# Kernel tuning notes

Measured on AMD Instinct MI355X. Metric: run time of the kernel, lower is better.

Reference implementation:

```python
import jax, jax.numpy as jnp
import numpy as np

N = 250_000    # total nodes across the batch of graphs
E = 2_000_000  # directed edges (no self loops)
F_IN = 3       # PROTEINS node feature dim
H = 32         # hid_channel
B = 128        # number of graphs in the batch


def _connected_components(u, v, n):
    """Weakly-connected components over selected edges via min-label propagation
    with pointer jumping. Final label = min node id in the component."""
    lab0 = jnp.arange(n, dtype=u.dtype)
    def body(state):
        lab, _ = state
        m = jnp.minimum(lab[u], lab[v])
        new = lab.at[u].min(m).at[v].min(m)
        new = jnp.minimum(new, new[new])  # pointer jumping
        return new, jnp.any(new != lab)
    lab, _ = jax.lax.while_loop(lambda s: s[1], body, (lab0, jnp.bool_(True)))
    return lab


def _gcn(h, src, dst, w, self_w, n):
    """GCN propagation D^-1/2 (A + I) D^-1/2 h with per-edge weights w and
    per-node self-loop weights self_w (gcn_norm with add_remaining_self_loops)."""
    deg = jax.ops.segment_sum(w, dst, num_segments=n) + self_w
    dis = jnp.where(deg > 0, jax.lax.rsqrt(jnp.maximum(deg, 1e-12)), 0.0)
    msg = jax.ops.segment_sum(h[src] * (dis[src] * dis[dst] * w)[:, None], dst, num_segments=n)
    return msg + h * (dis * dis * self_w)[:, None]


def _forward(x, W1, b1, w_pool, b_pool, W3, b3, Wf, bf, src, dst, batch):
    n = x.shape[0]
    ew = jnp.ones_like(src, dtype=x.dtype)
    sw = jnp.ones((n,), x.dtype)
    # conv1 + ReLU (dropout = identity in eval mode)
    x1 = jax.nn.relu(_gcn(x @ W1, src, dst, ew, sw, n) + b1)
    # ClusterPooling edge scores: sigmoid(Linear([x_i ; x_j]))
    h = x1.shape[1]
    score = jax.nn.sigmoid(x1[src] @ w_pool[:h] + x1[dst] @ w_pool[h:] + b_pool)
    sel = score > 0.5
    # contract selected edges -> clusters (unselected edges mapped to harmless (0,0))
    u = jax.lax.stop_gradient(jnp.where(sel, src, 0))
    v = jax.lax.stop_gradient(jnp.where(sel, dst, 0))
    lab = _connected_components(u, v, n)            # cluster id = representative (min) node id
    rep = lab == jnp.arange(n, dtype=lab.dtype)     # valid (non-empty) cluster slots
    repf = rep.astype(x.dtype)
    # cluster score = mean score of contracted edges; 1.0 for singleton clusters
    grp = lab[src]
    cnt = jax.ops.segment_sum(sel.astype(x.dtype), grp, num_segments=n)
    ssum = jax.ops.segment_sum(jnp.where(sel, score, jnp.zeros_like(score)), grp, num_segments=n)
    cscore = jnp.where(cnt > 0, ssum / jnp.maximum(cnt, 1.0), 1.0)
    # new cluster features = (sum of member features) * cluster score
    new_x = jax.ops.segment_sum(x1, lab, num_segments=n) * cscore[:, None]
    # relabel edges to cluster ids, coalesce (dedup) and drop self loops
    ru, rv = lab[src], lab[dst]
    order = jnp.lexsort((rv, ru))
    rus, rvs = ru[order], rv[order]
    first = jnp.concatenate([jnp.ones((1,), bool), (rus[1:] != rus[:-1]) | (rvs[1:] != rvs[:-1])])
    w = (first & (rus != rvs)).astype(x.dtype)
    # conv3 + ReLU on pooled graph (self loops only on valid cluster slots)
    x3 = jax.nn.relu(_gcn(new_x @ W3, rus, rvs, w, repf, n) + b3)
    # global mean pool over the clusters of each graph (invalid slots -> dummy seg B)
    seg = jnp.where(rep, batch, B)
    gs = jax.ops.segment_sum(x3 * repf[:, None], seg, num_segments=B + 1)[:B]
    gc = jax.ops.segment_sum(repf, seg, num_segments=B + 1)[:B]
    pooled = gs / jnp.maximum(gc, 1.0)[:, None]
    return jax.nn.sigmoid(pooled @ Wf + bf).reshape(-1)  # [B], binary task -> sigmoid + flatten


def setup_inputs() -> dict:
    key = jax.random.key(0)
    ks = jax.random.split(key, 10)
    x = jax.random.normal(ks[0], (N, F_IN), dtype=jnp.float32)
    src = jax.random.randint(ks[1], (E,), 0, N, dtype=jnp.int32)
    off = jax.random.randint(ks[2], (E,), 1, N, dtype=jnp.int32)
    dst = ((src + off) % N).astype(jnp.int32)  # no self loops
    edge_list = jnp.stack([src, dst], axis=1)  # [E, 2], forward transposes
    batch = jnp.sort(jax.random.randint(ks[3], (N,), 0, B, dtype=jnp.int32))
    W1 = jax.random.normal(ks[4], (F_IN, H), jnp.float32) * 0.5
    b1 = jnp.zeros((H,), jnp.float32)
    w_pool = jax.random.normal(ks[5], (2 * H,), jnp.float32) * 0.5
    b_pool = jnp.float32(-1.0)
    W3 = jax.random.normal(ks[6], (H, H), jnp.float32) * 0.3
    b3 = jnp.zeros((H,), jnp.float32)
    Wf = jax.random.normal(ks[7], (H, 1), jnp.float32) * 0.3
    bf = jnp.zeros((1,), jnp.float32)
    return dict(x=x, edge_list=edge_list, batch=batch, W1=W1, b1=b1,
                w_pool=w_pool, b_pool=b_pool, W3=W3, b3=b3, Wf=Wf, bf=bf)


def reference(x, edge_list, batch, W1, b1, w_pool, b_pool, W3, b3, Wf, bf):
    src, dst = edge_list[:, 0], edge_list[:, 1]
    return _forward(x, W1, b1, w_pool, b_pool, W3, b3, Wf, bf, src, dst, batch)
```

## Files before the change

### kernel.cpp

```cpp
#include <hip/hip_runtime.h>

typedef unsigned long long u64;
typedef unsigned int u32;

#define HF 32
#define TBL_BITS 22
#define TBL_SIZE (1u << TBL_BITS)
#define LP_ITERS 12
#define EMPTY_KEY 0xFFFFFFFFFFFFFFFFull
#define HSLOTS 256


__global__ void k_count(const int2* __restrict__ edges, int* __restrict__ cnt, int E) {
    int e = blockIdx.x * blockDim.x + threadIdx.x;
    if (e >= E) return;
    atomicAdd(&cnt[edges[e].y], 1);
}

__global__ void k_scan1(const int* __restrict__ cnt, int* __restrict__ row,
                        int* __restrict__ bsums, int N) {
    __shared__ int s[256];
    int tid = threadIdx.x;
    int i = blockIdx.x * 256 + tid;
    int v = (i < N) ? cnt[i] : 0;
    s[tid] = v;
    __syncthreads();
    for (int o = 1; o < 256; o <<= 1) {
        int t = (tid >= o) ? s[tid - o] : 0;
        __syncthreads();
        s[tid] += t;
        __syncthreads();
    }
    if (i < N) row[i] = s[tid] - v;
    if (tid == 255) bsums[blockIdx.x] = s[255];
}

__global__ void k_scan2(int* __restrict__ bsums, int nb) {
    __shared__ int s[1024];
    int tid = threadIdx.x;
    int v = (tid < nb) ? bsums[tid] : 0;
    s[tid] = v;
    __syncthreads();
    for (int o = 1; o < 1024; o <<= 1) {
        int t = (tid >= o) ? s[tid - o] : 0;
        __syncthreads();
        s[tid] += t;
        __syncthreads();
    }
    if (tid < nb) bsums[tid] = s[tid] - v;
}

__global__ void k_scan3(int* __restrict__ row, int* __restrict__ cursor,
                        const int* __restrict__ bsums, int N, int E) {
    int i = blockIdx.x * 256 + threadIdx.x;
    if (i < N) {
        int v = row[i] + bsums[blockIdx.x];
        row[i] = v;
        cursor[i] = v;
    }
    if (i == 0) row[N] = E;
}

__global__ void k_fill(const int2* __restrict__ edges, int* __restrict__ cursor,
                       int* __restrict__ csr_src, int E) {
    int e = blockIdx.x * blockDim.x + threadIdx.x;
    if (e >= E) return;
    int2 ed = edges[e];
    int pos = atomicAdd(&cursor[ed.y], 1);
    csr_src[pos] = ed.x;
}


__global__ void k_gather_x1(const int* __restrict__ row, const int* __restrict__ csr_src,
                            const float* __restrict__ x, const float* __restrict__ W1,
                            const float* __restrict__ b1, const float* __restrict__ wp,
                            float* __restrict__ x1, float* __restrict__ a_src,
                            float* __restrict__ a_dst, int* __restrict__ lab, int N) {
    __shared__ float w[96];
    __shared__ float wpl[64];
    __shared__ float b1l[32];
    int tid = threadIdx.x;
    if (tid < 96) w[tid] = W1[tid];
    if (tid < 64) wpl[tid] = wp[tid];
    if (tid < 32) b1l[tid] = b1[tid];
    __syncthreads();
    int t = blockIdx.x * blockDim.x + tid;
    int i = t >> 3, fg = t & 7;
    if (i >= N) return;
    int f = fg * 4;
    float wa0 = w[f + 0], wa1 = w[f + 1], wa2 = w[f + 2], wa3 = w[f + 3];
    float wb0 = w[32 + f + 0], wb1 = w[32 + f + 1], wb2 = w[32 + f + 2], wb3 = w[32 + f + 3];
    float wc0 = w[64 + f + 0], wc1 = w[64 + f + 1], wc2 = w[64 + f + 2], wc3 = w[64 + f + 3];
    int r0 = row[i], r1 = row[i + 1];
    float disI = rsqrtf((float)(r1 - r0) + 1.0f);
    float xi0 = x[3 * i + 0], xi1 = x[3 * i + 1], xi2 = x[3 * i + 2];
    float4 acc;
    acc.x = (xi0 * wa0 + xi1 * wb0 + xi2 * wc0) * disI;
    acc.y = (xi0 * wa1 + xi1 * wb1 + xi2 * wc1) * disI;
    acc.z = (xi0 * wa2 + xi1 * wb2 + xi2 * wc2) * disI;
    acc.w = (xi0 * wa3 + xi1 * wb3 + xi2 * wc3) * disI;
    for (int j = r0; j < r1; j++) {
        int s = csr_src[j];
        float s0 = x[3 * s + 0], s1 = x[3 * s + 1], s2 = x[3 * s + 2];
        int sr0 = row[s], sr1 = row[s + 1];
        float disS = rsqrtf((float)(sr1 - sr0) + 1.0f);
        acc.x += (s0 * wa0 + s1 * wb0 + s2 * wc0) * disS;
        acc.y += (s0 * wa1 + s1 * wb1 + s2 * wc1) * disS;
        acc.z += (s0 * wa2 + s1 * wb2 + s2 * wc2) * disS;
        acc.w += (s0 * wa3 + s1 * wb3 + s2 * wc3) * disS;
    }
    float4 r;
    r.x = fmaxf(disI * acc.x + b1l[f + 0], 0.0f);
    r.y = fmaxf(disI * acc.y + b1l[f + 1], 0.0f);
    r.z = fmaxf(disI * acc.z + b1l[f + 2], 0.0f);
    r.w = fmaxf(disI * acc.w + b1l[f + 3], 0.0f);
    ((float4*)x1)[i * 8 + fg] = r;
    float ps = r.x * wpl[f + 0] + r.y * wpl[f + 1] + r.z * wpl[f + 2] + r.w * wpl[f + 3];
    float pd = r.x * wpl[32 + f + 0] + r.y * wpl[32 + f + 1] + r.z * wpl[32 + f + 2] + r.w * wpl[32 + f + 3];
#pragma unroll
    for (int o = 4; o; o >>= 1) {
        ps += __shfl_xor(ps, o);
        pd += __shfl_xor(pd, o);
    }
    if (fg == 0) {
        a_src[i] = ps;
        a_dst[i] = pd;
        lab[i] = i;
    }
}


__global__ void k_select(const int2* __restrict__ edges, const float* __restrict__ a_src,
                         const float* __restrict__ a_dst, const float* __restrict__ bp,
                         long long* __restrict__ seluv, float* __restrict__ selsc,
                         int* __restrict__ selcnt, int E) {
    __shared__ int wsum[4];
    __shared__ int sbase;
    int tid = threadIdx.x;
    int e = blockIdx.x * 256 + tid;
    bool sel = false;
    long long pk = 0;
    float score = 0.0f;
    if (e < E) {
        int2 ed = edges[e];
        float z = a_src[ed.x] + a_dst[ed.y] + bp[0];
        score = 1.0f / (1.0f + expf(-z));
        if (score > 0.5f) {
            sel = true;
            pk = ((long long)ed.x << 32) | (u32)ed.y;
        }
    }
    u64 m = __ballot(sel);
    int wid = tid >> 6, lane = tid & 63;
    if (lane == 0) wsum[wid] = __popcll(m);
    __syncthreads();
    if (tid == 0) {
        int tot = wsum[0] + wsum[1] + wsum[2] + wsum[3];
        sbase = tot ? atomicAdd(selcnt, tot) : 0;
    }
    __syncthreads();
    if (sel) {
        int woff = 0;
        for (int k = 0; k < wid; k++) woff += wsum[k];
        int rank = __popcll(m & ((1ull << lane) - 1ull));
        int pos = sbase + woff + rank;
        seluv[pos] = pk;
        selsc[pos] = score;
    }
}


__global__ void k_lp(const long long* __restrict__ seluv, const int* __restrict__ pcnt,
                     int* __restrict__ lab, int* __restrict__ flags, int t, int N) {
    if (t > 0 && flags[t - 1] == 0) return;
    int n = *pcnt;
    int ch = 0;
    int tid0 = blockIdx.x * blockDim.x + threadIdx.x;
    int stride = gridDim.x * blockDim.x;
    for (int idx = tid0; idx < n; idx += stride) {
        long long pk = seluv[idx];
        int u = (int)(pk >> 32), v = (int)(u32)pk;
        int lu = lab[u], lv = lab[v];
        if (lu < lv) { atomicMin(&lab[v], lu); ch = 1; }
        else if (lv < lu) { atomicMin(&lab[u], lv); ch = 1; }
    }
    for (int i = tid0; i < N; i += stride) {
        int l = lab[i];
        int m = lab[l];
        int m2 = lab[m];
        if (m2 < l) { atomicMin(&lab[i], m2); ch = 1; }
    }
    if (__ballot(ch) && (int)(threadIdx.x & 63) == 0) flags[t] = 1;
}


__global__ void k_cnt_ssum(const long long* __restrict__ seluv, const float* __restrict__ selsc,
                           const int* __restrict__ pcnt, const int* __restrict__ lab,
                           float* __restrict__ cnt, float* __restrict__ ssum) {
    __shared__ int hkey[HSLOTS];
    __shared__ float hcnt[HSLOTS];
    __shared__ float hsum[HSLOTS];
    int tid = threadIdx.x;
    for (int k = tid; k < HSLOTS; k += 256) {
        hkey[k] = -1;
        hcnt[k] = 0.0f;
        hsum[k] = 0.0f;
    }
    __syncthreads();
    int n = *pcnt;
    for (int base = blockIdx.x * blockDim.x; base < n; base += gridDim.x * blockDim.x) {
        int idx = base + tid;
        bool valid = idx < n;
        int g = -1;
        float score = 0.0f;
        if (valid) {
            long long pk = seluv[idx];
            int s = (int)(pk >> 32);
            score = selsc[idx];
            g = lab[s];
        }
        u64 m = __ballot(valid);
        while (m) {
            int leader = __ffsll(m) - 1;
            int g0 = __shfl(g, leader);
            bool match = valid && (g == g0);
            float c = match ? 1.0f : 0.0f;
            float sv = match ? score : 0.0f;
#pragma unroll
            for (int o = 32; o; o >>= 1) {
                c += __shfl_xor(c, o);
                sv += __shfl_xor(sv, o);
            }
            if ((int)(tid & 63) == leader) {
                u32 h = ((u32)g0 * 0x9E3779B9u) >> 24;
                bool done = false;
                for (int probe = 0; probe < 16; probe++) {
                    int k = (int)((h + probe) & (HSLOTS - 1));
                    int prev = atomicCAS(&hkey[k], -1, g0);
                    if (prev == -1 || prev == g0) {
                        atomicAdd(&hcnt[k], c);
                        atomicAdd(&hsum[k], sv);
                        done = true;
                        break;
                    }
                }
                if (!done) {
                    atomicAdd(&cnt[g0], c);
                    atomicAdd(&ssum[g0], sv);
                }
            }
            m &= ~__ballot(match);
        }
    }
    __syncthreads();
    for (int k = tid; k < HSLOTS; k += 256) {
        int g = hkey[k];
        if (g >= 0) {
            atomicAdd(&cnt[g], hcnt[k]);
            atomicAdd(&ssum[g], hsum[k]);
        }
    }
}

__global__ void k_findgl(const float* __restrict__ cnt, u64* __restrict__ glpack, int N) {
    int i = blockIdx.x * blockDim.x + threadIdx.x;
    u64 v = 0;
    if (i < N) v = ((u64)__float_as_uint(cnt[i]) << 32) | (u32)i;
#pragma unroll
    for (int o = 32; o; o >>= 1) {
        u64 ov = __shfl_xor(v, o);
        v = v > ov ? v : ov;
    }
    if ((int)(threadIdx.x & 63) == 0) {
        if (*glpack < v) atomicMax(glpack, v);
    }
}

__global__ void k_nx_scatter(const float* __restrict__ x1, const int* __restrict__ lab,
                             const u64* __restrict__ glpack, float* __restrict__ nx, int N) {
    __shared__ float ls[HF];
    int tid = threadIdx.x;
    if (tid < HF) ls[tid] = 0.0f;
    __syncthreads();
    int gl = (int)(u32)(*glpack);
    int t = blockIdx.x * blockDim.x + tid;
    int i = t >> 3, fg = t & 7;
    if (i < N) {
        int l = lab[i];
        float4 v = ((const float4*)x1)[i * 8 + fg];
        if (l == gl) {
            atomicAdd(&ls[fg * 4 + 0], v.x);
            atomicAdd(&ls[fg * 4 + 1], v.y);
            atomicAdd(&ls[fg * 4 + 2], v.z);
            atomicAdd(&ls[fg * 4 + 3], v.w);
        } else {
            float* d = &nx[l * HF + fg * 4];
            atomicAdd(d + 0, v.x);
            atomicAdd(d + 1, v.y);
            atomicAdd(d + 2, v.z);
            atomicAdd(d + 3, v.w);
        }
    }
    __syncthreads();
    if (tid < HF) {
        float s = ls[tid];
        if (s != 0.0f) atomicAdd(&nx[gl * HF + tid], s);
    }
}


__global__ void k_hash_insert(const int2* __restrict__ edges, const int* __restrict__ lab,
                              u64* __restrict__ htab, float* __restrict__ deg3, int E) {
    int e = blockIdx.x * blockDim.x + threadIdx.x;
    if (e >= E) return;
    int2 ed = edges[e];
    int ru = lab[ed.x];
    int rv = lab[ed.y];
    if (ru == rv) return;
    u64 key = ((u64)(u32)ru << 32) | (u32)rv;
    u32 slot = (u32)((key * 0x9E3779B97F4A7C15ull) >> (64 - TBL_BITS));
    bool won = false;
    for (;;) {
        u64 cur = htab[slot];
        if (cur == key) break;
        if (cur == EMPTY_KEY) {
            u64 prev = atomicCAS(&htab[slot], EMPTY_KEY, key);
            if (prev == EMPTY_KEY) { won = true; break; }
            if (prev == key) break;
        }
        slot = (slot + 1) & (TBL_SIZE - 1);
    }
    if (won) atomicAdd(&deg3[rv], 1.0f);
}

__global__ void k_h3(const float* __restrict__ nx, const float* __restrict__ cnt,
                     const float* __restrict__ ssum, const float* __restrict__ deg3,
                     const int* __restrict__ lab, const float* __restrict__ W3,
                     float* __restrict__ hs3, float* __restrict__ dis3, int N) {
    __shared__ float w[HF * HF];
    int tid = threadIdx.x;
    for (int k = tid; k < HF * HF; k += blockDim.x) w[k] = W3[k];
    __syncthreads();
    int i = blockIdx.x * blockDim.x + tid;
    if (i >= N) return;
    if (lab[i] != i) {
        dis3[i] = 0.0f;
        return;
    }
    float cn = cnt[i];
    float c = cn > 0.0f ? ssum[i] / fmaxf(cn, 1.0f) : 1.0f;
    float d3 = 1.0f / sqrtf(deg3[i] + 1.0f);
    dis3[i] = d3;
    float scale = c * d3;
    float r[HF];
#pragma unroll
    for (int f = 0; f < HF; f++) r[f] = 0.0f;
    for (int k = 0; k < HF; k++) {
        float xv = nx[i * HF + k];
#pragma unroll
        for (int f = 0; f < HF; f++) r[f] += xv * w[k * HF + f];
    }
#pragma unroll
    for (int f = 0; f < HF; f++) hs3[i * HF + f] = r[f] * scale;
}

__global__ void k_hash_scatter(const u64* __restrict__ htab, const float* __restrict__ hs3,
                               float* __restrict__ acc3, const u64* __restrict__ glpack) {
    __shared__ float ls[HF];
    int tid = threadIdx.x;
    if (tid < HF) ls[tid] = 0.0f;
    __syncthreads();
    int gl = (int)(u32)(*glpack);
    int t = blockIdx.x * blockDim.x + tid;
    u32 slot = (u32)(t >> 3);
    int fg = t & 7;
    u64 key = htab[slot];
    if (key != EMPTY_KEY) {
        int a = (int)(key >> 32), b = (int)(u32)key;
        float4 v = ((const float4*)hs3)[a * 8 + fg];
        if (b == gl) {
            atomicAdd(&ls[fg * 4 + 0], v.x);
            atomicAdd(&ls[fg * 4 + 1], v.y);
            atomicAdd(&ls[fg * 4 + 2], v.z);
            atomicAdd(&ls[fg * 4 + 3], v.w);
        } else {
            float* d = &acc3[b * HF + fg * 4];
            atomicAdd(d + 0, v.x);
            atomicAdd(d + 1, v.y);
            atomicAdd(d + 2, v.z);
            atomicAdd(d + 3, v.w);
        }
    }
    __syncthreads();
    if (tid < HF) {
        float s = ls[tid];
        if (s != 0.0f) atomicAdd(&acc3[gl * HF + tid], s);
    }
}

__global__ void k_final(const float* __restrict__ acc3, const float* __restrict__ hs3,
                        const float* __restrict__ dis3, const int* __restrict__ lab,
                        const int* __restrict__ batch, const float* __restrict__ b3,
                        float* __restrict__ gs, float* __restrict__ gc, int N) {
    int t = blockIdx.x * blockDim.x + threadIdx.x;
    int i = t >> 3, fg = t & 7;
    if (i >= N) return;
    if (lab[i] != i) return;
    float d3 = dis3[i];
    float4 a = ((const float4*)acc3)[i * 8 + fg];
    float4 h = ((const float4*)hs3)[i * 8 + fg];
    int f = fg * 4;
    float4 x3;
    x3.x = fmaxf(d3 * (a.x + h.x) + b3[f + 0], 0.0f);
    x3.y = fmaxf(d3 * (a.y + h.y) + b3[f + 1], 0.0f);
    x3.z = fmaxf(d3 * (a.z + h.z) + b3[f + 2], 0.0f);
    x3.w = fmaxf(d3 * (a.w + h.w) + b3[f + 3], 0.0f);
    int b = batch[i];
    float* g = &gs[b * HF + f];
    atomicAdd(g + 0, x3.x);
    atomicAdd(g + 1, x3.y);
    atomicAdd(g + 2, x3.z);
    atomicAdd(g + 3, x3.w);
    if (fg == 0) atomicAdd(&gc[b], 1.0f);
}

__global__ void k_out(const float* __restrict__ gs, const float* __restrict__ gc,
                      const float* __restrict__ Wf, const float* __restrict__ bf,
                      float* __restrict__ out, int B) {
    int b = threadIdx.x + blockIdx.x * blockDim.x;
    if (b >= B) return;
    float inv = 1.0f / fmaxf(gc[b], 1.0f);
    float z = 0.0f;
#pragma unroll
    for (int f = 0; f < HF; f++) z += gs[b * HF + f] * inv * Wf[f];
    z += bf[0];
    out[b] = 1.0f / (1.0f + expf(-z));
}


static inline size_t align256(size_t x) { return (x + 255) & ~(size_t)255; }

extern "C" void kernel_launch(void* const* d_in, const int* in_sizes, int n_in,
                              void* d_out, int out_size, void* d_ws, size_t ws_size,
                              hipStream_t stream) {
    const float* x = (const float*)d_in[0];
    const int2* edges = (const int2*)d_in[1];
    const int* batch = (const int*)d_in[2];
    const float* W1 = (const float*)d_in[3];
    const float* b1 = (const float*)d_in[4];
    const float* wp = (const float*)d_in[5];
    const float* bp = (const float*)d_in[6];
    const float* W3 = (const float*)d_in[7];
    const float* b3 = (const float*)d_in[8];
    const float* Wf = (const float*)d_in[9];
    const float* bf = (const float*)d_in[10];
    float* outp = (float*)d_out;

    const int N = in_sizes[2];
    const int E = in_sizes[1] / 2;
    const int B = out_size;

    char* p = (char*)d_ws;
    size_t off = 0;
    auto alloc = [&](size_t bytes) -> void* {
        void* r = p + off;
        off = align256(off + bytes);
        return r;
    };
    float* f0 = (float*)alloc((size_t)N * HF * 4);
    float* f1 = (float*)alloc((size_t)N * HF * 4);
    int* row = (int*)alloc((size_t)(N + 1) * 4);
    int* cursor = (int*)alloc((size_t)N * 4);
    int* bsums = (int*)alloc(4096);
    int* csr_src = (int*)alloc((size_t)E * 4);
    float* a_src = (float*)alloc((size_t)N * 4);
    float* a_dst = (float*)alloc((size_t)N * 4);
    int* lab = (int*)alloc((size_t)N * 4);
    float* cnt = (float*)alloc((size_t)N * 4);
    float* ssum = (float*)alloc((size_t)N * 4);
    float* deg3 = (float*)alloc((size_t)N * 4);
    float* dis3 = (float*)alloc((size_t)N * 4);
    long long* seluv = (long long*)alloc((size_t)E * 8);
    float* selsc = (float*)alloc((size_t)E * 4);
    int* selcnt = (int*)alloc(4);
    int* flags = (int*)alloc(LP_ITERS * 4);
    u64* glpack = (u64*)alloc(8);
    float* gs = (float*)alloc((size_t)B * HF * 4);
    float* gc = (float*)alloc((size_t)B * 4);
    u64* htab = (u64*)alloc((size_t)TBL_SIZE * 8);
    (void)ws_size; (void)n_in;

    const int nb_e = (E + 255) / 256;
    const int nb_n8 = (int)(((size_t)N * 8 + 255) / 256);
    const int nb_n = (N + 255) / 256;
    const int nb_tbl8 = (int)(((size_t)TBL_SIZE * 8) / 256);

    hipMemsetAsync(cursor, 0, (size_t)N * 4, stream);
    hipMemsetAsync(cnt, 0, (size_t)N * 4, stream);
    hipMemsetAsync(ssum, 0, (size_t)N * 4, stream);
    hipMemsetAsync(deg3, 0, (size_t)N * 4, stream);
    hipMemsetAsync(selcnt, 0, 4, stream);
    hipMemsetAsync(flags, 0, LP_ITERS * 4, stream);
    hipMemsetAsync(glpack, 0, 8, stream);
    hipMemsetAsync(gs, 0, (size_t)B * HF * 4, stream);
    hipMemsetAsync(gc, 0, (size_t)B * 4, stream);
    hipMemsetAsync(htab, 0xFF, (size_t)TBL_SIZE * 8, stream);

    k_count<<<nb_e, 256, 0, stream>>>(edges, cursor, E);
    k_scan1<<<nb_n, 256, 0, stream>>>(cursor, row, bsums, N);
    k_scan2<<<1, 1024, 0, stream>>>(bsums, nb_n);
    k_scan3<<<nb_n, 256, 0, stream>>>(row, cursor, bsums, N, E);
    k_fill<<<nb_e, 256, 0, stream>>>(edges, cursor, csr_src, E);

    k_gather_x1<<<nb_n8, 256, 0, stream>>>(row, csr_src, x, W1, b1, wp, f1, a_src, a_dst, lab, N);

    k_select<<<nb_e, 256, 0, stream>>>(edges, a_src, a_dst, bp, seluv, selsc, selcnt, E);
    for (int t = 0; t < LP_ITERS; t++) {
        k_lp<<<2048, 256, 0, stream>>>(seluv, selcnt, lab, flags, t, N);
    }

    k_cnt_ssum<<<1024, 256, 0, stream>>>(seluv, selsc, selcnt, lab, cnt, ssum);
    k_findgl<<<nb_n, 256, 0, stream>>>(cnt, glpack, N);
    hipMemsetAsync(f0, 0, (size_t)N * HF * 4, stream);
    k_nx_scatter<<<nb_n8, 256, 0, stream>>>(f1, lab, glpack, f0, N);

    k_hash_insert<<<nb_e, 256, 0, stream>>>(edges, lab, htab, deg3, E);
    k_h3<<<nb_n, 256, 0, stream>>>(f0, cnt, ssum, deg3, lab, W3, f1, dis3, N);
    hipMemsetAsync(f0, 0, (size_t)N * HF * 4, stream);
    k_hash_scatter<<<nb_tbl8, 256, 0, stream>>>(htab, f1, f0, glpack);
    k_final<<<nb_n8, 256, 0, stream>>>(f0, f1, dis3, lab, batch, b3, gs, gc, N);
    k_out<<<1, 128, 0, stream>>>(gs, gc, Wf, bf, outp, B);
}
```

Baseline: 1.074 ms.

## Replace CSR gather for conv1 with atomic scatter of 3-dim inputs before projection

Drops the CSR build (scans plus fill) for the first GCN layer. Because the layer is linear, the normalized neighbor features are aggregated in the 3-wide input space with float atomics and multiplied by W1 afterwards, so each node's 8 feature-group threads no longer walk the neighbor list separately. This trades a serial per-node gather loop and four kernels for one edge-parallel kernel issuing 3 float atomics per edge. Float-atomic summation order is nondeterministic, which may shift results slightly.

```diff
diff --git a/kernel.cpp b/kernel.cpp
--- a/kernel.cpp
+++ b/kernel.cpp
@@ -11,71 +11,30 @@
 #define HSLOTS 256
 
 
-__global__ void k_count(const int2* __restrict__ edges, int* __restrict__ cnt, int E) {
+__global__ void k_count(const int2* __restrict__ edges, int* __restrict__ deg, int E) {
     int e = blockIdx.x * blockDim.x + threadIdx.x;
     if (e >= E) return;
-    atomicAdd(&cnt[edges[e].y], 1);
-}
-
-__global__ void k_scan1(const int* __restrict__ cnt, int* __restrict__ row,
-                        int* __restrict__ bsums, int N) {
-    __shared__ int s[256];
-    int tid = threadIdx.x;
-    int i = blockIdx.x * 256 + tid;
-    int v = (i < N) ? cnt[i] : 0;
-    s[tid] = v;
-    __syncthreads();
-    for (int o = 1; o < 256; o <<= 1) {
-        int t = (tid >= o) ? s[tid - o] : 0;
-        __syncthreads();
-        s[tid] += t;
-        __syncthreads();
-    }
-    if (i < N) row[i] = s[tid] - v;
-    if (tid == 255) bsums[blockIdx.x] = s[255];
-}
-
-__global__ void k_scan2(int* __restrict__ bsums, int nb) {
-    __shared__ int s[1024];
-    int tid = threadIdx.x;
-    int v = (tid < nb) ? bsums[tid] : 0;
-    s[tid] = v;
-    __syncthreads();
-    for (int o = 1; o < 1024; o <<= 1) {
-        int t = (tid >= o) ? s[tid - o] : 0;
-        __syncthreads();
-        s[tid] += t;
-        __syncthreads();
-    }
-    if (tid < nb) bsums[tid] = s[tid] - v;
-}
-
-__global__ void k_scan3(int* __restrict__ row, int* __restrict__ cursor,
-                        const int* __restrict__ bsums, int N, int E) {
-    int i = blockIdx.x * 256 + threadIdx.x;
-    if (i < N) {
-        int v = row[i] + bsums[blockIdx.x];
-        row[i] = v;
-        cursor[i] = v;
-    }
-    if (i == 0) row[N] = E;
-}
-
-__global__ void k_fill(const int2* __restrict__ edges, int* __restrict__ cursor,
-                       int* __restrict__ csr_src, int E) {
+    atomicAdd(&deg[edges[e].y], 1);
+}
+
+
+__global__ void k_scatter3(const int2* __restrict__ edges, const float* __restrict__ x,
+                           const int* __restrict__ deg, float* __restrict__ acc, int E) {
     int e = blockIdx.x * blockDim.x + threadIdx.x;
     if (e >= E) return;
     int2 ed = edges[e];
-    int pos = atomicAdd(&cursor[ed.y], 1);
-    csr_src[pos] = ed.x;
-}
-
-
-__global__ void k_gather_x1(const int* __restrict__ row, const int* __restrict__ csr_src,
-                            const float* __restrict__ x, const float* __restrict__ W1,
-                            const float* __restrict__ b1, const float* __restrict__ wp,
-                            float* __restrict__ x1, float* __restrict__ a_src,
-                            float* __restrict__ a_dst, int* __restrict__ lab, int N) {
+    float dis = rsqrtf((float)deg[ed.x] + 1.0f);
+    float* d = &acc[ed.y * 3];
+    atomicAdd(d + 0, x[3 * ed.x + 0] * dis);
+    atomicAdd(d + 1, x[3 * ed.x + 1] * dis);
+    atomicAdd(d + 2, x[3 * ed.x + 2] * dis);
+}
+
+__global__ void k_x1(const float* __restrict__ acc, const float* __restrict__ x,
+                     const int* __restrict__ deg, const float* __restrict__ W1,
+                     const float* __restrict__ b1, const float* __restrict__ wp,
+                     float* __restrict__ x1, float* __restrict__ a_src,
+                     float* __restrict__ a_dst, int* __restrict__ lab, int N) {
     __shared__ float w[96];
     __shared__ float wpl[64];
     __shared__ float b1l[32];
@@ -87,33 +46,16 @@
     int t = blockIdx.x * blockDim.x + tid;
     int i = t >> 3, fg = t & 7;
     if (i >= N) return;
+    float dis = rsqrtf((float)deg[i] + 1.0f);
+    float v0 = acc[3 * i + 0] + x[3 * i + 0] * dis;
+    float v1 = acc[3 * i + 1] + x[3 * i + 1] * dis;
+    float v2 = acc[3 * i + 2] + x[3 * i + 2] * dis;
     int f = fg * 4;
-    float wa0 = w[f + 0], wa1 = w[f + 1], wa2 = w[f + 2], wa3 = w[f + 3];
-    float wb0 = w[32 + f + 0], wb1 = w[32 + f + 1], wb2 = w[32 + f + 2], wb3 = w[32 + f + 3];
-    float wc0 = w[64 + f + 0], wc1 = w[64 + f + 1], wc2 = w[64 + f + 2], wc3 = w[64 + f + 3];
-    int r0 = row[i], r1 = row[i + 1];
-    float disI = rsqrtf((float)(r1 - r0) + 1.0f);
-    float xi0 = x[3 * i + 0], xi1 = x[3 * i + 1], xi2 = x[3 * i + 2];
-    float4 acc;
-    acc.x = (xi0 * wa0 + xi1 * wb0 + xi2 * wc0) * disI;
-    acc.y = (xi0 * wa1 + xi1 * wb1 + xi2 * wc1) * disI;
-    acc.z = (xi0 * wa2 + xi1 * wb2 + xi2 * wc2) * disI;
-    acc.w = (xi0 * wa3 + xi1 * wb3 + xi2 * wc3) * disI;
-    for (int j = r0; j < r1; j++) {
-        int s = csr_src[j];
-        float s0 = x[3 * s + 0], s1 = x[3 * s + 1], s2 = x[3 * s + 2];
-        int sr0 = row[s], sr1 = row[s + 1];
-        float disS = rsqrtf((float)(sr1 - sr0) + 1.0f);
-        acc.x += (s0 * wa0 + s1 * wb0 + s2 * wc0) * disS;
-        acc.y += (s0 * wa1 + s1 * wb1 + s2 * wc1) * disS;
-        acc.z += (s0 * wa2 + s1 * wb2 + s2 * wc2) * disS;
-        acc.w += (s0 * wa3 + s1 * wb3 + s2 * wc3) * disS;
-    }
     float4 r;
-    r.x = fmaxf(disI * acc.x + b1l[f + 0], 0.0f);
-    r.y = fmaxf(disI * acc.y + b1l[f + 1], 0.0f);
-    r.z = fmaxf(disI * acc.z + b1l[f + 2], 0.0f);
-    r.w = fmaxf(disI * acc.w + b1l[f + 3], 0.0f);
+    r.x = fmaxf(dis * (v0 * w[f + 0] + v1 * w[32 + f + 0] + v2 * w[64 + f + 0]) + b1l[f + 0], 0.0f);
+    r.y = fmaxf(dis * (v0 * w[f + 1] + v1 * w[32 + f + 1] + v2 * w[64 + f + 1]) + b1l[f + 1], 0.0f);
+    r.z = fmaxf(dis * (v0 * w[f + 2] + v1 * w[32 + f + 2] + v2 * w[64 + f + 2]) + b1l[f + 2], 0.0f);
+    r.w = fmaxf(dis * (v0 * w[f + 3] + v1 * w[32 + f + 3] + v2 * w[64 + f + 3]) + b1l[f + 3], 0.0f);
     ((float4*)x1)[i * 8 + fg] = r;
     float ps = r.x * wpl[f + 0] + r.y * wpl[f + 1] + r.z * wpl[f + 2] + r.w * wpl[f + 3];
     float pd = r.x * wpl[32 + f + 0] + r.y * wpl[32 + f + 1] + r.z * wpl[32 + f + 2] + r.w * wpl[32 + f + 3];
@@ -469,10 +411,8 @@
     };
     float* f0 = (float*)alloc((size_t)N * HF * 4);
     float* f1 = (float*)alloc((size_t)N * HF * 4);
-    int* row = (int*)alloc((size_t)(N + 1) * 4);
-    int* cursor = (int*)alloc((size_t)N * 4);
-    int* bsums = (int*)alloc(4096);
-    int* csr_src = (int*)alloc((size_t)E * 4);
+    int* deg = (int*)alloc((size_t)N * 4);
+    float* acc = (float*)alloc((size_t)N * 3 * 4);
     float* a_src = (float*)alloc((size_t)N * 4);
     float* a_dst = (float*)alloc((size_t)N * 4);
     int* lab = (int*)alloc((size_t)N * 4);
@@ -495,7 +435,8 @@
     const int nb_n = (N + 255) / 256;
     const int nb_tbl8 = (int)(((size_t)TBL_SIZE * 8) / 256);
 
-    hipMemsetAsync(cursor, 0, (size_t)N * 4, stream);
+    hipMemsetAsync(deg, 0, (size_t)N * 4, stream);
+    hipMemsetAsync(acc, 0, (size_t)N * 3 * 4, stream);
     hipMemsetAsync(cnt, 0, (size_t)N * 4, stream);
     hipMemsetAsync(ssum, 0, (size_t)N * 4, stream);
     hipMemsetAsync(deg3, 0, (size_t)N * 4, stream);
@@ -506,13 +447,9 @@
     hipMemsetAsync(gc, 0, (size_t)B * 4, stream);
     hipMemsetAsync(htab, 0xFF, (size_t)TBL_SIZE * 8, stream);
 
-    k_count<<<nb_e, 256, 0, stream>>>(edges, cursor, E);
-    k_scan1<<<nb_n, 256, 0, stream>>>(cursor, row, bsums, N);
-    k_scan2<<<1, 1024, 0, stream>>>(bsums, nb_n);
-    k_scan3<<<nb_n, 256, 0, stream>>>(row, cursor, bsums, N, E);
-    k_fill<<<nb_e, 256, 0, stream>>>(edges, cursor, csr_src, E);
-
-    k_gather_x1<<<nb_n8, 256, 0, stream>>>(row, csr_src, x, W1, b1, wp, f1, a_src, a_dst, lab, N);
+    k_count<<<nb_e, 256, 0, stream>>>(edges, deg, E);
+    k_scatter3<<<nb_e, 256, 0, stream>>>(edges, x, deg, acc, E);
+    k_x1<<<nb_n8, 256, 0, stream>>>(acc, x, deg, W1, b1, wp, f1, a_src, a_dst, lab, N);
 
     k_select<<<nb_e, 256, 0, stream>>>(edges, a_src, a_dst, bp, seluv, selsc, selcnt, E);
     for (int t = 0; t < LP_ITERS; t++) {
```

Result: slower. 1.169 ms (+8.8%).
